# Optimization experiments

Measured on AMD Instinct MI355X. Metric: run time of the kernel, lower is better.

Reference implementation:

```python
import jax, jax.numpy as jnp
import numpy as np


def setup_inputs() -> dict:
    key = jax.random.key(0)
    # values near 1 so a 4096-long cumulative product stays numerically sane
    x = 1.0 + 0.001 * jax.random.normal(key, (32, 4096, 512), dtype=jnp.float32)
    return {"x": x, "dim": 1}


def reference(x, dim):
    # cumulative product along `dim` (inclusive scan), same math as torch.cumprod
    return jnp.cumprod(x, axis=dim)
```

## Files before the change

### kernel.cpp

```cpp
#include <hip/hip_runtime.h>


constexpr int L  = 4096;
constexpr int C  = 512;
constexpr int C4 = C / 4;
constexpr int CG = 8;
constexpr int W  = 64;
constexpr int KE = 8;
constexpr int CL = W * KE;
constexpr int NCHUNK = L / CL;

__device__ __forceinline__ float4 mul4(float4 a, float4 b) {
    return make_float4(a.x * b.x, a.y * b.y, a.z * b.z, a.w * b.w);
}

__global__ __launch_bounds__(CG * W, 4)
void cumprod_kernel(const float4* __restrict__ x, float4* __restrict__ out) {
    __shared__ float4 s[W][CG + 1];

    const int tid = threadIdx.x;
    const int c4  = tid & (CG - 1);
    const int w   = tid >> 3;
    const int c4g = blockIdx.x * CG + c4;
    const int b   = blockIdx.y;

    const int base = (b * L) * C4 + c4g;

    float4 carry = make_float4(1.f, 1.f, 1.f, 1.f);

    for (int chunk = 0; chunk < NCHUNK; ++chunk) {
        const int lbase = base + (chunk * CL + w * KE) * C4;

        float4 v[KE];
#pragma unroll
        for (int i = 0; i < KE; ++i) v[i] = x[lbase + i * C4];

#pragma unroll
        for (int i = 1; i < KE; ++i) v[i] = mul4(v[i], v[i - 1]);

        s[w][c4] = v[KE - 1];
        __syncthreads();
#pragma unroll
        for (int d = 1; d < W; d <<= 1) {
            float4 t;
            bool act = (w >= d);
            if (act) t = s[w - d][c4];
            __syncthreads();
            if (act) s[w][c4] = mul4(s[w][c4], t);
            __syncthreads();
        }

        float4 excl = carry;
        if (w > 0) excl = mul4(excl, s[w - 1][c4]);
        const float4 total = s[W - 1][c4];

#pragma unroll
        for (int i = 0; i < KE; ++i) {
            out[lbase + i * C4] = mul4(excl, v[i]);
        }

        carry = mul4(carry, total);
        __syncthreads();
    }
}

extern "C" void kernel_launch(void* const* d_in, const int* in_sizes, int n_in,
                              void* d_out, int out_size, void* d_ws, size_t ws_size,
                              hipStream_t stream) {
    const float4* x = (const float4*)d_in[0];
    float4* out = (float4*)d_out;

    const int B = in_sizes[0] / (L * C);

    dim3 grid(C4 / CG, B);
    dim3 block(CG * W);
    cumprod_kernel<<<grid, block, 0, stream>>>(x, out);
}
```

Before: 458.5 us.

## Replace shared-memory block scan with wave shuffles and prefetch next chunk

The 64-step shared-memory Hillis-Steele scan, which needed two block barriers per step, is replaced by an intra-wave shuffle-up scan. A single barrier per chunk then combines the eight per-wave totals through a double-buffered shared array. The next chunk's loads are issued into registers before the current chunk is processed, and loads and stores use nontemporal hints. This removes most barriers and shared-memory traffic and overlaps memory latency, at the cost of extra registers for the prefetch buffer and a serial 8-way combine.

```diff
diff --git a/kernel.cpp b/kernel.cpp
--- a/kernel.cpp
+++ b/kernel.cpp
@@ -1,5 +1,7 @@
 #include <hip/hip_runtime.h>
 
+
+typedef float f4 __attribute__((ext_vector_type(4)));
 
 constexpr int L  = 4096;
 constexpr int C  = 512;
@@ -9,66 +11,95 @@
 constexpr int KE = 8;
 constexpr int CL = W * KE;
 constexpr int NCHUNK = L / CL;
+constexpr int NWAVE = CG * W / 64;
+constexpr int WPW = 64 / CG;
 
-__device__ __forceinline__ float4 mul4(float4 a, float4 b) {
-    return make_float4(a.x * b.x, a.y * b.y, a.z * b.z, a.w * b.w);
+__device__ __forceinline__ f4 shflup(f4 v, int lanes) {
+    f4 r;
+#pragma unroll
+    for (int j = 0; j < 4; ++j) r[j] = __shfl_up(v[j], lanes, 64);
+    return r;
 }
 
 __global__ __launch_bounds__(CG * W, 4)
-void cumprod_kernel(const float4* __restrict__ x, float4* __restrict__ out) {
-    __shared__ float4 s[W][CG + 1];
+void cumprod_kernel(const f4* __restrict__ x, f4* __restrict__ out) {
+    __shared__ f4 s[2][NWAVE][CG + 1];
 
-    const int tid = threadIdx.x;
-    const int c4  = tid & (CG - 1);
-    const int w   = tid >> 3;
-    const int c4g = blockIdx.x * CG + c4;
-    const int b   = blockIdx.y;
-
+    const int tid  = threadIdx.x;
+    const int c4   = tid & (CG - 1);
+    const int w    = tid >> 3;
+    const int lane = tid & 63;
+    const int wi   = lane >> 3;
+    const int ww   = tid >> 6;
+    const int c4g  = blockIdx.x * CG + c4;
+    const int b    = blockIdx.y;
     const int base = (b * L) * C4 + c4g;
 
-    float4 carry = make_float4(1.f, 1.f, 1.f, 1.f);
+    f4 carry = {1.f, 1.f, 1.f, 1.f};
+
+    f4 p[KE];
+    {
+        const int lb = base + (w * KE) * C4;
+#pragma unroll
+        for (int i = 0; i < KE; ++i)
+            p[i] = __builtin_nontemporal_load(&x[lb + i * C4]);
+    }
 
     for (int chunk = 0; chunk < NCHUNK; ++chunk) {
-        const int lbase = base + (chunk * CL + w * KE) * C4;
+        f4 v[KE];
+#pragma unroll
+        for (int i = 0; i < KE; ++i) v[i] = p[i];
 
-        float4 v[KE];
+        if (chunk + 1 < NCHUNK) {
+            const int lb = base + ((chunk + 1) * CL + w * KE) * C4;
 #pragma unroll
-        for (int i = 0; i < KE; ++i) v[i] = x[lbase + i * C4];
+            for (int i = 0; i < KE; ++i)
+                p[i] = __builtin_nontemporal_load(&x[lb + i * C4]);
+        }
 
 #pragma unroll
-        for (int i = 1; i < KE; ++i) v[i] = mul4(v[i], v[i - 1]);
+        for (int i = 1; i < KE; ++i) v[i] = v[i] * v[i - 1];
 
-        s[w][c4] = v[KE - 1];
-        __syncthreads();
+        f4 seg = v[KE - 1];
 #pragma unroll
-        for (int d = 1; d < W; d <<= 1) {
-            float4 t;
-            bool act = (w >= d);
-            if (act) t = s[w - d][c4];
-            __syncthreads();
-            if (act) s[w][c4] = mul4(s[w][c4], t);
-            __syncthreads();
+        for (int d = 1; d < WPW; d <<= 1) {
+            f4 t = shflup(seg, d * CG);
+            if (wi >= d) seg = seg * t;
         }
 
-        float4 excl = carry;
-        if (w > 0) excl = mul4(excl, s[w - 1][c4]);
-        const float4 total = s[W - 1][c4];
+        f4 exw = shflup(seg, CG);
 
+        if (wi == WPW - 1) s[chunk & 1][ww][c4] = seg;
+
+        asm volatile("s_waitcnt lgkmcnt(0)" ::: "memory");
+        __builtin_amdgcn_s_barrier();
+
+        f4 wpre = {1.f, 1.f, 1.f, 1.f};
+        f4 tot  = {1.f, 1.f, 1.f, 1.f};
 #pragma unroll
-        for (int i = 0; i < KE; ++i) {
-            out[lbase + i * C4] = mul4(excl, v[i]);
+        for (int j = 0; j < NWAVE; ++j) {
+            f4 sj = s[chunk & 1][j][c4];
+            if (j < ww) wpre = wpre * sj;
+            tot = tot * sj;
         }
 
-        carry = mul4(carry, total);
-        __syncthreads();
+        f4 pref = carry * wpre;
+        if (wi > 0) pref = pref * exw;
+
+        const int lb = base + (chunk * CL + w * KE) * C4;
+#pragma unroll
+        for (int i = 0; i < KE; ++i)
+            __builtin_nontemporal_store(pref * v[i], &out[lb + i * C4]);
+
+        carry = carry * tot;
     }
 }
 
 extern "C" void kernel_launch(void* const* d_in, const int* in_sizes, int n_in,
                               void* d_out, int out_size, void* d_ws, size_t ws_size,
                               hipStream_t stream) {
-    const float4* x = (const float4*)d_in[0];
-    float4* out = (float4*)d_out;
+    const f4* x = (const f4*)d_in[0];
+    f4* out = (f4*)d_out;
 
     const int B = in_sizes[0] / (L * C);
 
```

After: 449.0 us. -2.1%, faster.
